# Optimization experiments

Measured on AMD Instinct MI355X. Metric: run time of the kernel, lower is better.

Reference implementation:

```python
import jax, jax.numpy as jnp
import numpy as np

B, T, D, H = 4, 2048, 2048, 16
HD = D // H

def setup_inputs() -> dict:
    key = jax.random.key(0)
    k1, k2, k3 = jax.random.split(key, 3)
    x = jax.random.normal(k1, (B, T, D), dtype=jnp.float32)
    mask = jnp.ones((B, T), dtype=jnp.int32)
    # torch Linear weights, scaled like default init (~1/sqrt(fan_in))
    w_qkv = jax.random.normal(k2, (3 * D, D), dtype=jnp.float32) / np.sqrt(D)
    w_o = jax.random.normal(k3, (D, D), dtype=jnp.float32) / np.sqrt(D)
    return {"x": x, "mask": mask, "w_qkv": w_qkv, "w_o": w_o}

def reference(x, mask, w_qkv, w_o):
    # qkv projection: (B,T,D) @ (D,3D) -> (B,T,3D)
    qkv = jnp.einsum('btd,ed->bte', x, w_qkv)
    q, k, v = jnp.split(qkv, 3, axis=-1)
    # (B,T,D) -> (B,H,T,HD)
    def to_heads(t):
        return t.reshape(B, T, H, HD).transpose(0, 2, 1, 3)
    q, k, v = to_heads(q), to_heads(k), to_heads(v)
    scale = 1.0 / np.sqrt(HD).astype(np.float32)
    att = jnp.einsum('bhqd,bhkd->bhqk', q, k) * scale  # (B,H,T,T)
    att = jnp.where(mask[:, None, None, :] == 0, -jnp.inf, att)
    att = jax.nn.softmax(att, axis=-1)
    y = jnp.einsum('bhqk,bhkd->bhqd', att, v)  # (B,H,T,HD)
    y = y.transpose(0, 2, 1, 3).reshape(B, T, D)
    return jnp.einsum('btd,ed->bte', y, w_o)
```

## Files before the change

### kernel.cpp

```cpp
#include <hip/hip_runtime.h>
#include <hip/hip_bf16.h>

typedef __bf16 bf16;
typedef bf16 bf16x8 __attribute__((ext_vector_type(8)));
typedef float f32x4 __attribute__((ext_vector_type(4)));

struct alignas(8) bh4 { bf16 v[4]; };

__device__ __forceinline__ void glds16(const bf16* g, bf16* l) {
  __builtin_amdgcn_global_load_lds(
      (const __attribute__((address_space(1))) void*)g,
      (__attribute__((address_space(3))) void*)l, 16, 0, 0);
}

#define QSCALE (1.4426950408889634f / 11.313708498984761f)
#define DEFER_THR 8.0f

__global__ void convert_to_bf16(const float* __restrict__ s, bf16* __restrict__ dst,
                                long n) {
  const long stride = (long)gridDim.x * blockDim.x * 8;
  for (long i = ((long)blockIdx.x * blockDim.x + threadIdx.x) * 8; i < n; i += stride) {
    float4 a = *(const float4*)(s + i);
    float4 b = *(const float4*)(s + i + 4);
    bf16x8 o;
    o[0] = (bf16)a.x; o[1] = (bf16)a.y; o[2] = (bf16)a.z; o[3] = (bf16)a.w;
    o[4] = (bf16)b.x; o[5] = (bf16)b.y; o[6] = (bf16)b.z; o[7] = (bf16)b.w;
    *(bf16x8*)(dst + i) = o;
  }
}

template <int MODE>
__global__ __launch_bounds__(512, 2)
void gemm256(const bf16* __restrict__ A, const bf16* __restrict__ Bw,
             void* __restrict__ C0v, bf16* __restrict__ C1,
             bf16* __restrict__ C2, int M, int N, int K) {
  __shared__ __align__(16) bf16 sA[2][256 * 64];
  __shared__ __align__(16) bf16 sB[2][256 * 64];
  const int tid = threadIdx.x;
  const int lane = tid & 63;
  const int wid = tid >> 6;
  const int wm = wid >> 2, wn = wid & 3;
  const int quad = lane >> 4, l16 = lane & 15;

  const int gx = gridDim.x;
  const int nwg = gx * gridDim.y;
  const int bid0 = blockIdx.y * gx + blockIdx.x;
  const int cpx = nwg >> 3;
  const int bid = (bid0 & 7) * cpx + (bid0 >> 3);
  const int bm = (bid / gx) * 256, bn = (bid % gx) * 256;

  f32x4 acc[8][4] = {};

#pragma unroll
  for (int r = 0; r < 4; ++r) {
    const int idx = r * 512 + tid;
    const int row = idx >> 3, cp = idx & 7;
    const int cs = cp ^ (row & 7);
    glds16(A + (size_t)(bm + row) * K + cs * 8, &sA[0][idx * 8]);
    glds16(Bw + (size_t)(bn + row) * K + cs * 8, &sB[0][idx * 8]);
  }
  asm volatile("s_waitcnt vmcnt(0)" ::: "memory");
  __builtin_amdgcn_s_barrier();

  const int NT = K >> 6;
  for (int kt = 0; kt < NT; ++kt) {
    const bf16* cA = sA[kt & 1];
    const bf16* cB = sB[kt & 1];
    bf16x8 af[4][2];
    bf16x8 bfA[2][2], bfB[2][2];

#pragma unroll
    for (int mt = 0; mt < 4; ++mt) {
      const int R = wm * 128 + mt * 16 + l16;
#pragma unroll
      for (int s = 0; s < 2; ++s)
        af[mt][s] = *(const bf16x8*)&cA[R * 64 + (((s * 4 + quad) ^ (R & 7)) * 8)];
    }
#pragma unroll
    for (int nt = 0; nt < 2; ++nt) {
      const int R = wn * 64 + nt * 16 + l16;
#pragma unroll
      for (int s = 0; s < 2; ++s)
        bfA[nt][s] = *(const bf16x8*)&cB[R * 64 + (((s * 4 + quad) ^ (R & 7)) * 8)];
    }
    if (kt + 1 < NT) {
      bf16* nA = (bf16*)sA[(kt + 1) & 1];
      bf16* nB = (bf16*)sB[(kt + 1) & 1];
      const int k0 = (kt + 1) << 6;
#pragma unroll
      for (int r = 0; r < 4; ++r) {
        const int idx = r * 512 + tid;
        const int row = idx >> 3, cp = idx & 7;
        const int cs = cp ^ (row & 7);
        glds16(A + (size_t)(bm + row) * K + k0 + cs * 8, &nA[idx * 8]);
        glds16(Bw + (size_t)(bn + row) * K + k0 + cs * 8, &nB[idx * 8]);
      }
    }
    __builtin_amdgcn_s_barrier();
    asm volatile("s_waitcnt lgkmcnt(0)" ::: "memory");
    __builtin_amdgcn_sched_barrier(0);
    __builtin_amdgcn_s_setprio(1);
#pragma unroll
    for (int mt = 0; mt < 4; ++mt)
#pragma unroll
      for (int nt = 0; nt < 2; ++nt)
#pragma unroll
        for (int s = 0; s < 2; ++s)
          acc[mt][nt] = __builtin_amdgcn_mfma_f32_16x16x32_bf16(af[mt][s], bfA[nt][s], acc[mt][nt], 0, 0, 0);
    __builtin_amdgcn_s_setprio(0);
    __builtin_amdgcn_s_barrier();

#pragma unroll
    for (int nt = 0; nt < 2; ++nt) {
      const int R = wn * 64 + (2 + nt) * 16 + l16;
#pragma unroll
      for (int s = 0; s < 2; ++s)
        bfB[nt][s] = *(const bf16x8*)&cB[R * 64 + (((s * 4 + quad) ^ (R & 7)) * 8)];
    }
    __builtin_amdgcn_s_barrier();
    asm volatile("s_waitcnt lgkmcnt(0)" ::: "memory");
    __builtin_amdgcn_sched_barrier(0);
    __builtin_amdgcn_s_setprio(1);
#pragma unroll
    for (int mt = 0; mt < 4; ++mt)
#pragma unroll
      for (int nt = 0; nt < 2; ++nt)
#pragma unroll
        for (int s = 0; s < 2; ++s)
          acc[mt][2 + nt] = __builtin_amdgcn_mfma_f32_16x16x32_bf16(af[mt][s], bfB[nt][s], acc[mt][2 + nt], 0, 0, 0);
    __builtin_amdgcn_s_setprio(0);
    __builtin_amdgcn_s_barrier();

#pragma unroll
    for (int mt = 0; mt < 4; ++mt) {
      const int R = wm * 128 + 64 + mt * 16 + l16;
#pragma unroll
      for (int s = 0; s < 2; ++s)
        af[mt][s] = *(const bf16x8*)&cA[R * 64 + (((s * 4 + quad) ^ (R & 7)) * 8)];
    }
    __builtin_amdgcn_s_barrier();
    asm volatile("s_waitcnt lgkmcnt(0)" ::: "memory");
    __builtin_amdgcn_sched_barrier(0);
    __builtin_amdgcn_s_setprio(1);
#pragma unroll
    for (int mt = 0; mt < 4; ++mt)
#pragma unroll
      for (int nt = 0; nt < 2; ++nt)
#pragma unroll
        for (int s = 0; s < 2; ++s)
          acc[4 + mt][nt] = __builtin_amdgcn_mfma_f32_16x16x32_bf16(af[mt][s], bfA[nt][s], acc[4 + mt][nt], 0, 0, 0);
    __builtin_amdgcn_s_setprio(0);
    __builtin_amdgcn_s_barrier();

    __builtin_amdgcn_s_setprio(1);
#pragma unroll
    for (int mt = 0; mt < 4; ++mt)
#pragma unroll
      for (int nt = 0; nt < 2; ++nt)
#pragma unroll
        for (int s = 0; s < 2; ++s)
          acc[4 + mt][2 + nt] = __builtin_amdgcn_mfma_f32_16x16x32_bf16(af[mt][s], bfB[nt][s], acc[4 + mt][2 + nt], 0, 0, 0);
    __builtin_amdgcn_s_setprio(0);
    asm volatile("s_waitcnt vmcnt(0)" ::: "memory");
    __builtin_amdgcn_s_barrier();
  }

  if (MODE == 0) {
    bf16* C0 = (bf16*)C0v;
#pragma unroll
    for (int i = 0; i < 8; ++i) {
      const int m0 = bm + wm * 128 + i * 16 + quad * 4;
      const int b = m0 >> 11, t0 = m0 & 2047;
#pragma unroll
      for (int j = 0; j < 4; ++j) {
        const int ncol = bn + wn * 64 + j * 16 + l16;
        const int which = ncol >> 11;
        const int d = ncol & 2047;
        const int h = d >> 7, hd = d & 127;
        if (which == 0) {
          bf16* dst = C0 + (((size_t)(b * 16 + h) * 2048 + t0) * 128 + hd);
#pragma unroll
          for (int r = 0; r < 4; ++r) dst[(size_t)r * 128] = (bf16)(acc[i][j][r] * QSCALE);
        } else if (which == 1) {
          bf16* dst = C1 + (((size_t)(b * 16 + h) * 2048 + t0) * 128 + hd);
#pragma unroll
          for (int r = 0; r < 4; ++r) dst[(size_t)r * 128] = (bf16)acc[i][j][r];
        } else {
          bh4 pk;
#pragma unroll
          for (int r = 0; r < 4; ++r) pk.v[r] = (bf16)acc[i][j][r];
          *(bh4*)(C2 + ((size_t)((b * 16 + h) * 128 + hd) * 2048 + t0)) = pk;
        }
      }
    }
  } else {
    float* C0 = (float*)C0v;
#pragma unroll
    for (int i = 0; i < 8; ++i) {
      const int m0 = bm + wm * 128 + i * 16 + quad * 4;
#pragma unroll
      for (int j = 0; j < 4; ++j) {
        const int n = bn + wn * 64 + j * 16 + l16;
#pragma unroll
        for (int r = 0; r < 4; ++r)
          C0[(size_t)(m0 + r) * N + n] = acc[i][j][r];
      }
    }
  }
}

__global__ __launch_bounds__(256, 3)
void attn_kernel(const bf16* __restrict__ Q, const bf16* __restrict__ Kb,
                 const bf16* __restrict__ Vt, const int* __restrict__ mask,
                 bf16* __restrict__ Y) {
  __shared__ __align__(16) bf16 smem[25600];
  bf16* sK = smem;
  bf16* sV = smem + 8192;
  bf16* sP = smem + 16384;

  const int tid = threadIdx.x;
  const int lane = tid & 63, w = tid >> 6;
  const int quad = lane >> 4, l16 = lane & 15;
  const int bh = blockIdx.x, b = bh >> 4, h = bh & 15;
  const int qt = blockIdx.y;
  const size_t head = (size_t)bh * (2048 * 128);

  bf16x8 qf[2][4];
#pragma unroll
  for (int nt = 0; nt < 2; ++nt) {
    const int t = qt * 128 + w * 32 + nt * 16 + l16;
    const bf16* g = Q + head + (size_t)t * 128 + quad * 8;
#pragma unroll
    for (int kk = 0; kk < 4; ++kk)
      qf[nt][kk] = *(const bf16x8*)(g + kk * 32);
  }

  f32x4 o[8][2] = {};
  float mrow[2] = {-3.0e38f, -3.0e38f};
  float lrow[2] = {0.0f, 0.0f};

  const int* maskb = mask + b * 2048;
  bf16* sPw = sP + w * (32 * 72);

  unsigned long long vmask;
  {
    const int4* mp4 = (const int4*)maskb;
    bool ok = true;
#pragma unroll
    for (int j = 0; j < 8; ++j) {
      const int4 q4 = mp4[lane * 8 + j];
      ok = ok && (q4.x != 0) && (q4.y != 0) && (q4.z != 0) && (q4.w != 0);
    }
    vmask = __ballot(ok);
  }

  for (int kt = 0; kt < 32; ++kt) {
    const int key0 = kt * 64;
    {
      const int cp = lane & 15;
      const int rbase = w * 16 + (lane >> 4);
#pragma unroll
      for (int p = 0; p < 4; ++p) {
        const int row = rbase + p * 4;
        const int c = (cp & 8) | ((cp ^ row) & 7);
        glds16(Kb + head + (size_t)(key0 + row) * 128 + c * 8,
               &sK[(w * 16 + p * 4) * 128 + lane * 8]);
      }
    }
    {
      const int cp = lane & 7;
      const int rbase = w * 32 + (lane >> 3);
#pragma unroll
      for (int p = 0; p < 4; ++p) {
        const int row = rbase + p * 8;
        const int c = cp ^ (row & 7);
        glds16(Vt + head + (size_t)row * 2048 + key0 + c * 8,
               &sV[(w * 32 + p * 8) * 64 + lane * 8]);
      }
    }
    __syncthreads();

    f32x4 st[4][2] = {};
#pragma unroll
    for (int kk = 0; kk < 4; ++kk) {
      bf16x8 ak[4];
#pragma unroll
      for (int mt = 0; mt < 4; ++mt) {
        const int row = mt * 16 + l16;
        const int c = kk * 4 + quad;
        const int cp = (c & 8) | ((c ^ row) & 7);
        ak[mt] = *(const bf16x8*)&sK[row * 128 + cp * 8];
      }
#pragma unroll
      for (int mt = 0; mt < 4; ++mt)
#pragma unroll
        for (int nt = 0; nt < 2; ++nt)
          st[mt][nt] = __builtin_amdgcn_mfma_f32_16x16x32_bf16(ak[mt], qf[nt][kk], st[mt][nt], 0, 0, 0);
    }

    if (((vmask >> (2 * kt)) & 3ULL) != 3ULL) {
#pragma unroll
      for (int mt = 0; mt < 4; ++mt) {
#pragma unroll
        for (int r = 0; r < 4; ++r) {
          const int mk = maskb[key0 + mt * 16 + quad * 4 + r];
#pragma unroll
          for (int nt = 0; nt < 2; ++nt)
            if (mk == 0) { st[mt][nt][r] = -1.0e30f; }
        }
      }
    }

#pragma unroll
    for (int nt = 0; nt < 2; ++nt) {
      float mx = -1.0e30f;
#pragma unroll
      for (int mt = 0; mt < 4; ++mt)
#pragma unroll
        for (int r = 0; r < 4; ++r) mx = fmaxf(mx, st[mt][nt][r]);
      mx = fmaxf(mx, __shfl_xor(mx, 16));
      mx = fmaxf(mx, __shfl_xor(mx, 32));
      if (!__all(mx <= mrow[nt] + DEFER_THR)) {
        const float newm = fmaxf(mrow[nt], mx);
        const float alpha = exp2f(mrow[nt] - newm);
        mrow[nt] = newm;
        lrow[nt] *= alpha;
#pragma unroll
        for (int mt = 0; mt < 8; ++mt)
#pragma unroll
          for (int r = 0; r < 4; ++r) o[mt][nt][r] *= alpha;
      }
      const float m = mrow[nt];
      float rs = 0.0f;
#pragma unroll
      for (int mt = 0; mt < 4; ++mt) {
        bh4 pk;
#pragma unroll
        for (int r = 0; r < 4; ++r) {
          const float p = exp2f(st[mt][nt][r] - m);
          rs += p;
          pk.v[r] = (bf16)p;
        }
        *(bh4*)&sPw[(nt * 16 + l16) * 72 + mt * 16 + quad * 4] = pk;
      }
      rs += __shfl_xor(rs, 16);
      rs += __shfl_xor(rs, 32);
      lrow[nt] += rs;
    }

#pragma unroll
    for (int kk = 0; kk < 2; ++kk) {
      bf16x8 bp[2];
#pragma unroll
      for (int nt = 0; nt < 2; ++nt)
        bp[nt] = *(const bf16x8*)&sPw[(nt * 16 + l16) * 72 + kk * 32 + quad * 8];
#pragma unroll
      for (int mt = 0; mt < 8; ++mt) {
        const int row = mt * 16 + l16;
        const int c = kk * 4 + quad;
        bf16x8 av = *(const bf16x8*)&sV[row * 64 + (c ^ (row & 7)) * 8];
#pragma unroll
        for (int nt = 0; nt < 2; ++nt)
          o[mt][nt] = __builtin_amdgcn_mfma_f32_16x16x32_bf16(av, bp[nt], o[mt][nt], 0, 0, 0);
      }
    }
    __syncthreads();
  }

  bf16* sOw = smem + w * 4352;
#pragma unroll
  for (int nt = 0; nt < 2; ++nt) {
    const float inv = 1.0f / lrow[nt];
#pragma unroll
    for (int mt = 0; mt < 8; ++mt) {
      bh4 pk;
#pragma unroll
      for (int r = 0; r < 4; ++r) pk.v[r] = (bf16)(o[mt][nt][r] * inv);
      *(bh4*)&sOw[(nt * 16 + l16) * 136 + mt * 16 + quad * 4] = pk;
    }
  }
  {
    const int col = (lane & 15) * 8;
#pragma unroll
    for (int p = 0; p < 8; ++p) {
      const int row = p * 4 + (lane >> 4);
      int4 v = *(const int4*)&sOw[row * 136 + col];
      const int token = qt * 128 + w * 32 + row;
      *(int4*)(Y + ((size_t)(b * 2048 + token)) * 2048 + h * 128 + col) = v;
    }
  }
}

extern "C" void kernel_launch(void* const* d_in, const int* in_sizes, int n_in,
                              void* d_out, int out_size, void* d_ws, size_t ws_size,
                              hipStream_t stream) {
  const float* x_raw  = (const float*)d_in[0];
  const int*   mask   = (const int*)d_in[1];
  const float* wq_raw = (const float*)d_in[2];
  const float* wo_raw = (const float*)d_in[3];
  float* out = (float*)d_out;

  char* ws = (char*)d_ws;
  const size_t MB = 1024 * 1024;
  bf16* xb  = (bf16*)(ws + 256);
  bf16* wqb = (bf16*)(ws + 256 + 32 * MB);
  bf16* qb  = (bf16*)(ws + 256 + 56 * MB);
  bf16* kb  = (bf16*)(ws + 256 + 88 * MB);
  bf16* vt  = (bf16*)(ws + 256 + 120 * MB);
  bf16* yb  = xb;
  bf16* wob = wqb;

  convert_to_bf16<<<1024, 256, 0, stream>>>(x_raw, xb, (long)in_sizes[0]);
  convert_to_bf16<<<1024, 256, 0, stream>>>(wq_raw, wqb, (long)in_sizes[2]);

  gemm256<0><<<dim3(24, 32), 512, 0, stream>>>(xb, wqb, qb, kb, vt, 8192, 6144, 2048);

  convert_to_bf16<<<1024, 256, 0, stream>>>(wo_raw, wob, (long)in_sizes[3]);

  attn_kernel<<<dim3(64, 16), 256, 0, stream>>>(qb, kb, vt, mask, yb);

  gemm256<1><<<dim3(8, 32), 512, 0, stream>>>(yb, wob, out, nullptr, nullptr, 8192, 2048, 2048);
}
```

Baseline: 632.5 us.

## Split GEMM LDS tiles into halves and prefetch two k-tiles ahead

Each A and B shared-memory tile is split into two 128-row halves. Loads are issued per half, interleaved between the MFMA phases, and run up to two k-tiles ahead. The end-of-iteration wait now uses vmcnt(6) instead of vmcnt(0), so global loads stay in flight across iterations instead of draining every k-step. In exchange the buffer-reuse ordering and the barriers become more intricate, and one extra barrier is added per iteration.

```diff
diff --git a/kernel.cpp b/kernel.cpp
--- a/kernel.cpp
+++ b/kernel.cpp
@@ -34,8 +34,8 @@
 void gemm256(const bf16* __restrict__ A, const bf16* __restrict__ Bw,
              void* __restrict__ C0v, bf16* __restrict__ C1,
              bf16* __restrict__ C2, int M, int N, int K) {
-  __shared__ __align__(16) bf16 sA[2][256 * 64];
-  __shared__ __align__(16) bf16 sB[2][256 * 64];
+  __shared__ __align__(16) bf16 sA[2][2][128 * 64];
+  __shared__ __align__(16) bf16 sB[2][2][128 * 64];
   const int tid = threadIdx.x;
   const int lane = tid & 63;
   const int wid = tid >> 6;
@@ -51,51 +51,55 @@
 
   f32x4 acc[8][4] = {};
 
-#pragma unroll
-  for (int r = 0; r < 4; ++r) {
-    const int idx = r * 512 + tid;
-    const int row = idx >> 3, cp = idx & 7;
-    const int cs = cp ^ (row & 7);
-    glds16(A + (size_t)(bm + row) * K + cs * 8, &sA[0][idx * 8]);
-    glds16(Bw + (size_t)(bn + row) * K + cs * 8, &sB[0][idx * 8]);
-  }
-  asm volatile("s_waitcnt vmcnt(0)" ::: "memory");
+  const int s_r = tid >> 3;
+  const int s_cs = ((tid & 7) ^ (s_r & 7)) * 8;
+  const int grB0 = ((s_r >> 5) << 6) + (s_r & 31);
+
+  auto stageA = [&](int bufi, int hh, int ktile) {
+    const int k0 = ktile << 6;
+    bf16* dst = &sA[bufi][hh][0] + tid * 8;
+    const bf16* src = A + (size_t)(bm + hh * 64 + s_r) * K + k0 + s_cs;
+    glds16(src, dst);
+    glds16(src + (size_t)128 * K, dst + 4096);
+  };
+  auto stageB = [&](int bufi, int hh, int ktile) {
+    const int k0 = ktile << 6;
+    bf16* dst = &sB[bufi][hh][0] + tid * 8;
+    const bf16* src = Bw + (size_t)(bn + hh * 32 + grB0) * K + k0 + s_cs;
+    glds16(src, dst);
+    glds16(src + (size_t)128 * K, dst + 4096);
+  };
+
+  const int NT = K >> 6;
+  stageA(0, 0, 0);
+  stageB(0, 0, 0);
+  stageB(0, 1, 0);
+  stageA(0, 1, 0);
+  stageA(1, 0, 1);
+  stageB(1, 0, 1);
+  stageB(1, 1, 1);
+  asm volatile("s_waitcnt vmcnt(6)" ::: "memory");
   __builtin_amdgcn_s_barrier();
 
-  const int NT = K >> 6;
   for (int kt = 0; kt < NT; ++kt) {
-    const bf16* cA = sA[kt & 1];
-    const bf16* cB = sB[kt & 1];
-    bf16x8 af[4][2];
-    bf16x8 bfA[2][2], bfB[2][2];
+    const int buf = kt & 1;
+    bf16x8 af[4][2], bfA[2][2], bfB[2][2];
 
 #pragma unroll
     for (int mt = 0; mt < 4; ++mt) {
-      const int R = wm * 128 + mt * 16 + l16;
+      const int lr = wm * 64 + mt * 16 + l16;
 #pragma unroll
       for (int s = 0; s < 2; ++s)
-        af[mt][s] = *(const bf16x8*)&cA[R * 64 + (((s * 4 + quad) ^ (R & 7)) * 8)];
+        af[mt][s] = *(const bf16x8*)&sA[buf][0][lr * 64 + (((s * 4 + quad) ^ (lr & 7)) * 8)];
     }
 #pragma unroll
     for (int nt = 0; nt < 2; ++nt) {
-      const int R = wn * 64 + nt * 16 + l16;
+      const int lr = wn * 32 + nt * 16 + l16;
 #pragma unroll
       for (int s = 0; s < 2; ++s)
-        bfA[nt][s] = *(const bf16x8*)&cB[R * 64 + (((s * 4 + quad) ^ (R & 7)) * 8)];
-    }
-    if (kt + 1 < NT) {
-      bf16* nA = (bf16*)sA[(kt + 1) & 1];
-      bf16* nB = (bf16*)sB[(kt + 1) & 1];
-      const int k0 = (kt + 1) << 6;
-#pragma unroll
-      for (int r = 0; r < 4; ++r) {
-        const int idx = r * 512 + tid;
-        const int row = idx >> 3, cp = idx & 7;
-        const int cs = cp ^ (row & 7);
-        glds16(A + (size_t)(bm + row) * K + k0 + cs * 8, &nA[idx * 8]);
-        glds16(Bw + (size_t)(bn + row) * K + k0 + cs * 8, &nB[idx * 8]);
-      }
-    }
+        bfA[nt][s] = *(const bf16x8*)&sB[buf][0][lr * 64 + (((s * 4 + quad) ^ (lr & 7)) * 8)];
+    }
+    if (kt + 1 < NT) stageA(buf ^ 1, 1, kt + 1);
     __builtin_amdgcn_s_barrier();
     asm volatile("s_waitcnt lgkmcnt(0)" ::: "memory");
     __builtin_amdgcn_sched_barrier(0);
@@ -112,11 +116,12 @@
 
 #pragma unroll
     for (int nt = 0; nt < 2; ++nt) {
-      const int R = wn * 64 + (2 + nt) * 16 + l16;
+      const int lr = wn * 32 + nt * 16 + l16;
 #pragma unroll
       for (int s = 0; s < 2; ++s)
-        bfB[nt][s] = *(const bf16x8*)&cB[R * 64 + (((s * 4 + quad) ^ (R & 7)) * 8)];
-    }
+        bfB[nt][s] = *(const bf16x8*)&sB[buf][1][lr * 64 + (((s * 4 + quad) ^ (lr & 7)) * 8)];
+    }
+    if (kt + 2 < NT) stageA(buf, 0, kt + 2);
     __builtin_amdgcn_s_barrier();
     asm volatile("s_waitcnt lgkmcnt(0)" ::: "memory");
     __builtin_amdgcn_sched_barrier(0);
@@ -133,11 +138,12 @@
 
 #pragma unroll
     for (int mt = 0; mt < 4; ++mt) {
-      const int R = wm * 128 + 64 + mt * 16 + l16;
+      const int lr = wm * 64 + mt * 16 + l16;
 #pragma unroll
       for (int s = 0; s < 2; ++s)
-        af[mt][s] = *(const bf16x8*)&cA[R * 64 + (((s * 4 + quad) ^ (R & 7)) * 8)];
-    }
+        af[mt][s] = *(const bf16x8*)&sA[buf][1][lr * 64 + (((s * 4 + quad) ^ (lr & 7)) * 8)];
+    }
+    if (kt + 2 < NT) stageB(buf, 0, kt + 2);
     __builtin_amdgcn_s_barrier();
     asm volatile("s_waitcnt lgkmcnt(0)" ::: "memory");
     __builtin_amdgcn_sched_barrier(0);
@@ -152,6 +158,8 @@
     __builtin_amdgcn_s_setprio(0);
     __builtin_amdgcn_s_barrier();
 
+    if (kt + 2 < NT) stageB(buf, 1, kt + 2);
+    __builtin_amdgcn_s_barrier();
     __builtin_amdgcn_s_setprio(1);
 #pragma unroll
     for (int mt = 0; mt < 4; ++mt)
@@ -161,8 +169,11 @@
         for (int s = 0; s < 2; ++s)
           acc[4 + mt][2 + nt] = __builtin_amdgcn_mfma_f32_16x16x32_bf16(af[mt][s], bfB[nt][s], acc[4 + mt][2 + nt], 0, 0, 0);
     __builtin_amdgcn_s_setprio(0);
-    asm volatile("s_waitcnt vmcnt(0)" ::: "memory");
-    __builtin_amdgcn_s_barrier();
+    if (kt < NT - 1) {
+      if (kt < NT - 2) asm volatile("s_waitcnt vmcnt(6)" ::: "memory");
+      else             asm volatile("s_waitcnt vmcnt(0)" ::: "memory");
+      __builtin_amdgcn_s_barrier();
+    }
   }
 
   if (MODE == 0) {
```

After: 606.5 us. -4.1%, faster.
